# Kernel optimization log

Measured on AMD Instinct MI355X. Metric: run time of the kernel, lower is better.

The kernel has to match this reference:

```python
import jax, jax.numpy as jnp
import numpy as np

LAYERS = 3       # opt.layer
B = 4096         # batch of sessions
MAX_LEN = 200    # padded session length
N_ITEMS = 100000 # item vocab (index 0 is PAD after zero-row concat)
E = 112          # emb_size (SessConv default)
EPS = 1e-12      # F.normalize eps


def setup_inputs() -> dict:
    key = jax.random.key(0)
    k0, k1, k2, k3, k4 = jax.random.split(key, 5)
    item_embedding = jax.random.normal(k0, (N_ITEMS, E), dtype=jnp.float32) * 0.1
    # Session-session adjacency A and diagonal inverse-degree D (so D @ A is row-normalized)
    A = jax.random.uniform(k1, (B, B), dtype=jnp.float32)
    D = jnp.diag(1.0 / A.sum(axis=1))
    # Padded session item indices; 0 == PAD row (zeros prepended to the table)
    session_item = jax.random.randint(k2, (B, MAX_LEN), 0, N_ITEMS + 1, dtype=jnp.int64)
    session_len = jax.random.randint(k3, (B, 1), 1, MAX_LEN + 1).astype(jnp.float32)
    # layers x Linear(E, E, bias=False) weights, torch layout [out, in]
    Ws = jax.random.normal(k4, (LAYERS, E, E), dtype=jnp.float32) * (1.0 / np.sqrt(E))
    return {"item_embedding": item_embedding, "D": D, "A": A,
            "session_len": session_len, "Ws": Ws, "session_item": session_item}


def reference(item_embedding, D, A, session_len, Ws, session_item):
    # Prepend zero row so index 0 gathers zeros (padding)
    emb = jnp.concatenate([jnp.zeros((1, E), item_embedding.dtype), item_embedding], axis=0)
    # Fused ragged gather + mean-pool (replaces per-session index_select + cpu/numpy roundtrip)
    seq_h = emb[session_item]                       # [B, MAX_LEN, E]
    session_emb = seq_h.sum(axis=1) / session_len   # [B, E]
    DA = D @ A                                      # [B, B]
    acc = session_emb                               # layer-0 term of the final average
    for i in range(LAYERS):
        session_emb = session_emb @ Ws[i].T         # Linear(E,E,bias=False)
        session_emb = DA @ session_emb              # session graph propagation
        nrm = jnp.linalg.norm(session_emb, axis=-1, keepdims=True)
        acc = acc + session_emb / jnp.maximum(nrm, EPS)  # appended term is L2-normalized
        # NOTE: next layer consumes the UN-normalized session_emb (as in the torch code)
    return acc / (LAYERS + 1)
```

## Files before the change

### kernel.cpp

```cpp
#include <hip/hip_runtime.h>
#include <hip/hip_bf16.h>

#define BSZ 4096
#define MAXLEN 200
#define EDIM 112
#define NPL 8

typedef __attribute__((ext_vector_type(8))) short bf16x8;
typedef __attribute__((ext_vector_type(4))) float f32x4;

static __device__ __forceinline__ short f2bf(float f) {
    unsigned u = __float_as_uint(f);
    unsigned r = (u + 0x7fffu + ((u >> 16) & 1u)) >> 16;
    return (short)r;
}
static __device__ __forceinline__ float bf2f(short s) {
    return __uint_as_float(((unsigned)(unsigned short)s) << 16);
}
static __device__ __forceinline__ bf16x8 cvt8(float4 a, float4 b) {
    bf16x8 r;
    r[0] = f2bf(a.x); r[1] = f2bf(a.y); r[2] = f2bf(a.z); r[3] = f2bf(a.w);
    r[4] = f2bf(b.x); r[5] = f2bf(b.y); r[6] = f2bf(b.z); r[7] = f2bf(b.w);
    return r;
}
static __device__ __forceinline__ unsigned pack2(float a, float b) {
    return ((unsigned)f2bf(a) & 0xffffu) | ((unsigned)f2bf(b) << 16);
}

static __device__ __forceinline__ void glds16(const unsigned short* g, unsigned short* l) {
    __builtin_amdgcn_global_load_lds(
        (__attribute__((address_space(1))) void*)(void*)g,
        (__attribute__((address_space(3))) void*)l, 16, 0, 0);
}

__global__ __launch_bounds__(256) void f32_to_bf16(const float* __restrict__ src,
                                                   unsigned short* __restrict__ dst,
                                                   int ngroups, int zgroups) {
    int g = blockIdx.x * 256 + threadIdx.x;
    if (g >= ngroups) return;
    bf16x8 o;
    if (g < zgroups) {
        #pragma unroll
        for (int i = 0; i < 8; ++i) o[i] = 0;
    } else {
        const float* p = src + (size_t)(g - zgroups) * 8;
        float4 a = *(const float4*)p;
        float4 b = *(const float4*)(p + 4);
        o = cvt8(a, b);
    }
    *(bf16x8*)(dst + (size_t)g * 8) = o;
}

__global__ __launch_bounds__(256) void gather_pool_bf(const unsigned short* __restrict__ Ebf,
                                                      const int* __restrict__ items,
                                                      const float* __restrict__ slen,
                                                      float* __restrict__ S,
                                                      float* __restrict__ acc) {
    __shared__ float part[16][14][8];
    int wave = threadIdx.x >> 6;
    int lane = threadIdx.x & 63;
    int b = blockIdx.x;
    int rg = lane / 14;
    int c  = lane % 14;
    const int* it = items + (size_t)b * MAXLEN + wave * 50;
    float a[8];
    #pragma unroll
    for (int e = 0; e < 8; ++e) a[e] = 0.f;
    if (lane < 56) {
        #pragma unroll
        for (int t = 0; t < 13; ++t) {
            int j = t * 4 + rg;
            int idx = 0;
            if (j < 50) idx = it[j];
            bf16x8 v = *(const bf16x8*)(Ebf + (size_t)idx * EDIM + c * 8);
            #pragma unroll
            for (int e = 0; e < 8; ++e) a[e] += bf2f(v[e]);
        }
        #pragma unroll
        for (int e = 0; e < 8; ++e) part[wave * 4 + rg][c][e] = a[e];
    }
    __syncthreads();
    int tid = threadIdx.x;
    if (tid < EDIM) {
        int cc = tid >> 3, ee = tid & 7;
        float s = 0.f;
        #pragma unroll
        for (int g = 0; g < 16; ++g) s += part[g][cc][ee];
        s /= slen[b];
        S[(size_t)b * EDIM + tid]   = s;
        acc[(size_t)b * EDIM + tid] = s;
    }
}

static __device__ __forceinline__ bf16x8 ldcvt(const float* p, bool valid) {
    if (valid) {
        float4 a = *(const float4*)(p);
        float4 b = *(const float4*)(p + 4);
        return cvt8(a, b);
    }
    bf16x8 z;
    #pragma unroll
    for (int i = 0; i < 8; ++i) z[i] = 0;
    return z;
}

__global__ __launch_bounds__(64, 4) void fused_mid0(const float* __restrict__ Sin,
                                                    const float* __restrict__ W,
                                                    unsigned short* __restrict__ Bsw) {
    __shared__ unsigned short Ylds[16][136];
    int lane = threadIdx.x;
    int gw = blockIdx.x;
    int j0 = gw * 16;
    int nrow = lane & 15;
    int quad = lane >> 4;
    int ses = j0 + nrow;

    float4 v[7];
    const float4* p = (const float4*)(Sin + (size_t)ses * EDIM + quad * 28);
    #pragma unroll
    for (int i = 0; i < 7; ++i) v[i] = p[i];

    #pragma unroll
    for (int i = 0; i < 7; ++i) {
        uint2 pk;
        pk.x = pack2(v[i].x, v[i].y);
        pk.y = pack2(v[i].z, v[i].w);
        *(uint2*)&Ylds[nrow][quad * 28 + i * 4] = pk;
    }
    *(uint2*)&Ylds[nrow][112 + quad * 4] = make_uint2(0u, 0u);
    __syncthreads();

    bf16x8 aF[4];
    #pragma unroll
    for (int k32 = 0; k32 < 4; ++k32)
        aF[k32] = *(bf16x8*)&Ylds[nrow][k32 * 32 + quad * 8];

    f32x4 acc[7];
    #pragma unroll
    for (int t = 0; t < 7; ++t) acc[t] = (f32x4){0.f, 0.f, 0.f, 0.f};
    #pragma unroll
    for (int t = 0; t < 7; ++t) {
        const float* wr = W + (size_t)(16 * t + nrow) * EDIM;
        #pragma unroll
        for (int k32 = 0; k32 < 4; ++k32) {
            bf16x8 bF = ldcvt(wr + k32 * 32 + quad * 8, (k32 < 3) || (quad < 2));
            acc[t] = __builtin_amdgcn_mfma_f32_16x16x32_bf16(aF[k32], bF, acc[t], 0, 0, 0);
        }
    }

    int k32f = j0 >> 5;
    int qp = ((j0 >> 4) & 1) * 2 + (quad >> 1);
    int e0 = (quad & 1) * 4;
    #pragma unroll
    for (int t = 0; t < 7; ++t) {
        uint2 pk;
        pk.x = pack2(acc[t][0], acc[t][1]);
        pk.y = pack2(acc[t][2], acc[t][3]);
        *(uint2*)(Bsw + ((size_t)(k32f * 7 + t) * 64 + qp * 16 + nrow) * 8 + e0) = pk;
    }
}

template <int AMODE>
__global__ __launch_bounds__(512, 2) void bg_ks(const float* __restrict__ Af,
                                                unsigned short* __restrict__ Asw,
                                                const unsigned short* __restrict__ Bsw,
                                                float* __restrict__ Yp) {
    __shared__ unsigned short Bl[8 * 7 * 512];
    int tid = threadIdx.x;
    int w = tid >> 6;
    int lane = tid & 63;
    int nrow = lane & 15;
    int quad = lane >> 4;
    int mtile = blockIdx.x & 31;
    int kq = blockIdx.x >> 5;
    int M16 = mtile * 8 + w;
    int k32b = kq * 16;

    #pragma unroll
    for (int t = 0; t < 7; ++t)
        glds16(Bsw + (((size_t)(k32b + w) * 7 + t) * 64 + lane) * 8,
               &Bl[(w * 7 + t) * 512]);

    bf16x8 aF[16];
    if (AMODE == 0) {
        #pragma unroll
        for (int k = 0; k < 16; ++k) {
            const float* p = Af + (size_t)(M16 * 16 + nrow) * BSZ
                             + (k32b + k) * 32 + quad * 8;
            float4 a0 = *(const float4*)p;
            float4 a1 = *(const float4*)(p + 4);
            aF[k] = cvt8(a0, a1);
            *(bf16x8*)(Asw + (((size_t)M16 * 128 + k32b + k) * 64 + lane) * 8) = aF[k];
        }
    } else {
        #pragma unroll
        for (int k = 0; k < 16; ++k)
            aF[k] = *(const bf16x8*)(Asw + (((size_t)M16 * 128 + k32b + k) * 64 + lane) * 8);
    }

    f32x4 acc[7];
    #pragma unroll
    for (int t = 0; t < 7; ++t) acc[t] = (f32x4){0.f, 0.f, 0.f, 0.f};

    asm volatile("s_waitcnt vmcnt(0)" ::: "memory");
    __syncthreads();

    #pragma unroll
    for (int k = 0; k < 8; ++k)
        #pragma unroll
        for (int t = 0; t < 7; ++t) {
            bf16x8 bF = *(bf16x8*)&Bl[(k * 7 + t) * 512 + lane * 8];
            acc[t] = __builtin_amdgcn_mfma_f32_16x16x32_bf16(aF[k], bF, acc[t], 0, 0, 0);
        }

    __syncthreads();
    #pragma unroll
    for (int t = 0; t < 7; ++t)
        glds16(Bsw + (((size_t)(k32b + 8 + w) * 7 + t) * 64 + lane) * 8,
               &Bl[(w * 7 + t) * 512]);
    asm volatile("s_waitcnt vmcnt(0)" ::: "memory");
    __syncthreads();

    #pragma unroll
    for (int k = 0; k < 8; ++k)
        #pragma unroll
        for (int t = 0; t < 7; ++t) {
            bf16x8 bF = *(bf16x8*)&Bl[(k * 7 + t) * 512 + lane * 8];
            acc[t] = __builtin_amdgcn_mfma_f32_16x16x32_bf16(aF[8 + k], bF, acc[t], 0, 0, 0);
        }

    float* dst = Yp + (size_t)kq * BSZ * EDIM + (size_t)M16 * 16 * EDIM;
    #pragma unroll
    for (int t = 0; t < 7; ++t)
        #pragma unroll
        for (int r = 0; r < 4; ++r)
            dst[(size_t)(quad * 4 + r) * EDIM + 16 * t + nrow] = acc[t][r];
}

__global__ __launch_bounds__(64, 4) void epi_mid(const float* __restrict__ Yp,
                                                 const float* __restrict__ Dm,
                                                 float* __restrict__ accb,
                                                 const float* __restrict__ W,
                                                 unsigned short* __restrict__ Bsw) {
    __shared__ unsigned short Ylds[16][136];
    int lane = threadIdx.x;
    int gw = blockIdx.x;
    int j0 = gw * 16;
    int nrow = lane & 15;
    int quad = lane >> 4;
    int ses = j0 + nrow;

    float4 v[7];
    #pragma unroll
    for (int i = 0; i < 7; ++i) v[i] = make_float4(0.f, 0.f, 0.f, 0.f);
    #pragma unroll
    for (int pp = 0; pp < NPL; ++pp) {
        const float4* p = (const float4*)(Yp + (size_t)pp * BSZ * EDIM
                                          + (size_t)ses * EDIM + quad * 28);
        #pragma unroll
        for (int i = 0; i < 7; ++i) {
            float4 t = p[i];
            v[i].x += t.x; v[i].y += t.y; v[i].z += t.z; v[i].w += t.w;
        }
    }
    float d = Dm[(size_t)ses * (BSZ + 1)];
    float ss = 0.f;
    #pragma unroll
    for (int i = 0; i < 7; ++i) {
        v[i].x *= d; v[i].y *= d; v[i].z *= d; v[i].w *= d;
        ss += v[i].x * v[i].x + v[i].y * v[i].y + v[i].z * v[i].z + v[i].w * v[i].w;
    }
    ss += __shfl_xor(ss, 16, 64);
    ss += __shfl_xor(ss, 32, 64);
    float rinv = 1.f / fmaxf(sqrtf(ss), 1e-12f);
    float4* pa = (float4*)(accb + (size_t)ses * EDIM + quad * 28);
    #pragma unroll
    for (int i = 0; i < 7; ++i) {
        float4 a = pa[i];
        a.x += v[i].x * rinv; a.y += v[i].y * rinv;
        a.z += v[i].z * rinv; a.w += v[i].w * rinv;
        pa[i] = a;
    }

    #pragma unroll
    for (int i = 0; i < 7; ++i) {
        uint2 pk;
        pk.x = pack2(v[i].x, v[i].y);
        pk.y = pack2(v[i].z, v[i].w);
        *(uint2*)&Ylds[nrow][quad * 28 + i * 4] = pk;
    }
    *(uint2*)&Ylds[nrow][112 + quad * 4] = make_uint2(0u, 0u);
    __syncthreads();

    bf16x8 aF[4];
    #pragma unroll
    for (int k32 = 0; k32 < 4; ++k32)
        aF[k32] = *(bf16x8*)&Ylds[nrow][k32 * 32 + quad * 8];

    f32x4 acc[7];
    #pragma unroll
    for (int t = 0; t < 7; ++t) acc[t] = (f32x4){0.f, 0.f, 0.f, 0.f};
    #pragma unroll
    for (int t = 0; t < 7; ++t) {
        const float* wr = W + (size_t)(16 * t + nrow) * EDIM;
        #pragma unroll
        for (int k32 = 0; k32 < 4; ++k32) {
            bf16x8 bF = ldcvt(wr + k32 * 32 + quad * 8, (k32 < 3) || (quad < 2));
            acc[t] = __builtin_amdgcn_mfma_f32_16x16x32_bf16(aF[k32], bF, acc[t], 0, 0, 0);
        }
    }

    int k32f = j0 >> 5;
    int qp = ((j0 >> 4) & 1) * 2 + (quad >> 1);
    int e0 = (quad & 1) * 4;
    #pragma unroll
    for (int t = 0; t < 7; ++t) {
        uint2 pk;
        pk.x = pack2(acc[t][0], acc[t][1]);
        pk.y = pack2(acc[t][2], acc[t][3]);
        *(uint2*)(Bsw + ((size_t)(k32f * 7 + t) * 64 + qp * 16 + nrow) * 8 + e0) = pk;
    }
}

__global__ __launch_bounds__(256) void final_epilogue(const float* __restrict__ Yp,
                                                      const float* __restrict__ Dm,
                                                      const float* __restrict__ accb,
                                                      float* __restrict__ out) {
    int wave = threadIdx.x >> 6;
    int lane = threadIdx.x & 63;
    int b = blockIdx.x * 4 + wave;

    float2 v = make_float2(0.f, 0.f);
    size_t o2 = (size_t)b * 56 + lane;
    if (lane < 56) {
        #pragma unroll
        for (int p = 0; p < NPL; ++p) {
            float2 t = ((const float2*)(Yp + (size_t)p * BSZ * EDIM))[o2];
            v.x += t.x;
            v.y += t.y;
        }
    }
    float d = Dm[(size_t)b * (BSZ + 1)];
    v.x *= d; v.y *= d;
    float ss = v.x * v.x + v.y * v.y;
    #pragma unroll
    for (int off = 32; off; off >>= 1) ss += __shfl_xor(ss, off, 64);
    float nrm = fmaxf(sqrtf(ss), 1e-12f);
    if (lane < 56) {
        float2 a = ((const float2*)accb)[o2];
        ((float2*)out)[o2] = make_float2((a.x + v.x / nrm) * 0.25f,
                                         (a.y + v.y / nrm) * 0.25f);
    }
}

extern "C" void kernel_launch(void* const* d_in, const int* in_sizes, int n_in,
                              void* d_out, int out_size, void* d_ws, size_t ws_size,
                              hipStream_t stream) {
    (void)in_sizes; (void)n_in; (void)out_size; (void)ws_size;
    const float* emb   = (const float*)d_in[0];
    const float* Dm    = (const float*)d_in[1];
    const float* A     = (const float*)d_in[2];
    const float* slen  = (const float*)d_in[3];
    const float* Ws    = (const float*)d_in[4];
    const int*   items = (const int*)d_in[5];
    float* out = (float*)d_out;

    char* w = (char*)d_ws;
    float* Sa   = (float*)w;
    float* accb = Sa + BSZ * EDIM;
    float* Yp   = accb + BSZ * EDIM;
    unsigned short* Bsw0 = (unsigned short*)(Yp + (size_t)NPL * BSZ * EDIM);
    unsigned short* Bsw1 = Bsw0 + (size_t)128 * 7 * 64 * 8;
    unsigned short* Ebf  = Bsw1 + (size_t)128 * 7 * 64 * 8;
    unsigned short* Asw  = Ebf + (size_t)100001 * EDIM;

    f32_to_bf16<<<5470, 256, 0, stream>>>(emb, Ebf, 1400014, 14);
    gather_pool_bf<<<BSZ, 256, 0, stream>>>(Ebf, items, slen, Sa, accb);
    fused_mid0<<<256, 64, 0, stream>>>(Sa, Ws, Bsw0);
    bg_ks<0><<<256, 512, 0, stream>>>(A, Asw, Bsw0, Yp);
    epi_mid<<<256, 64, 0, stream>>>(Yp, Dm, accb, Ws + (size_t)EDIM * EDIM, Bsw1);
    bg_ks<1><<<256, 512, 0, stream>>>(nullptr, Asw, Bsw1, Yp);
    epi_mid<<<256, 64, 0, stream>>>(Yp, Dm, accb, Ws + (size_t)2 * EDIM * EDIM, Bsw0);
    bg_ks<1><<<256, 512, 0, stream>>>(nullptr, Asw, Bsw0, Yp);
    final_epilogue<<<BSZ / 4, 256, 0, stream>>>(Yp, Dm, accb, out);
}
```

Before: 274.3 us.

## Fuse layer kernels into one persistent kernel with grid-wide atomic barriers

Merges the weight-projection, the three graph-propagation GEMMs, the mid-layer epilogues and the final epilogue into a single persistent kernel of 256 blocks. Stages are separated by a software grid barrier built on an atomic counter. The intent is to remove the launch gaps and the tail idle time between seven small kernels. In exchange it relies on all 256 blocks being co-resident, otherwise it deadlocks, and it adds a memset plus spin-wait overhead at each barrier. The epilogue now runs on one wave per block instead of many small blocks.

```diff
diff --git a/kernel.cpp b/kernel.cpp
--- a/kernel.cpp
+++ b/kernel.cpp
@@ -5,6 +5,7 @@
 #define MAXLEN 200
 #define EDIM 112
 #define NPL 8
+#define NBLK 256
 
 typedef __attribute__((ext_vector_type(8))) short bf16x8;
 typedef __attribute__((ext_vector_type(4))) float f32x4;
@@ -31,6 +32,19 @@
     __builtin_amdgcn_global_load_lds(
         (__attribute__((address_space(1))) void*)(void*)g,
         (__attribute__((address_space(3))) void*)l, 16, 0, 0);
+}
+
+static __device__ __forceinline__ void gsync(unsigned* cnt, unsigned idx) {
+    __syncthreads();
+    if (threadIdx.x == 0) {
+        __threadfence();
+        __hip_atomic_fetch_add(cnt, 1u, __ATOMIC_RELEASE, __HIP_MEMORY_SCOPE_AGENT);
+        while (__hip_atomic_load(cnt, __ATOMIC_ACQUIRE, __HIP_MEMORY_SCOPE_AGENT)
+               < idx * (unsigned)NBLK)
+            __builtin_amdgcn_s_sleep(2);
+        __threadfence();
+    }
+    __syncthreads();
 }
 
 __global__ __launch_bounds__(256) void f32_to_bf16(const float* __restrict__ src,
@@ -104,252 +118,226 @@
     return z;
 }
 
-__global__ __launch_bounds__(64, 4) void fused_mid0(const float* __restrict__ Sin,
-                                                    const float* __restrict__ W,
-                                                    unsigned short* __restrict__ Bsw) {
-    __shared__ unsigned short Ylds[16][136];
-    int lane = threadIdx.x;
-    int gw = blockIdx.x;
-    int j0 = gw * 16;
-    int nrow = lane & 15;
-    int quad = lane >> 4;
-    int ses = j0 + nrow;
-
-    float4 v[7];
-    const float4* p = (const float4*)(Sin + (size_t)ses * EDIM + quad * 28);
-    #pragma unroll
-    for (int i = 0; i < 7; ++i) v[i] = p[i];
-
-    #pragma unroll
-    for (int i = 0; i < 7; ++i) {
-        uint2 pk;
-        pk.x = pack2(v[i].x, v[i].y);
-        pk.y = pack2(v[i].z, v[i].w);
-        *(uint2*)&Ylds[nrow][quad * 28 + i * 4] = pk;
-    }
-    *(uint2*)&Ylds[nrow][112 + quad * 4] = make_uint2(0u, 0u);
-    __syncthreads();
-
-    bf16x8 aF[4];
-    #pragma unroll
-    for (int k32 = 0; k32 < 4; ++k32)
-        aF[k32] = *(bf16x8*)&Ylds[nrow][k32 * 32 + quad * 8];
-
-    f32x4 acc[7];
-    #pragma unroll
-    for (int t = 0; t < 7; ++t) acc[t] = (f32x4){0.f, 0.f, 0.f, 0.f};
-    #pragma unroll
-    for (int t = 0; t < 7; ++t) {
-        const float* wr = W + (size_t)(16 * t + nrow) * EDIM;
-        #pragma unroll
-        for (int k32 = 0; k32 < 4; ++k32) {
-            bf16x8 bF = ldcvt(wr + k32 * 32 + quad * 8, (k32 < 3) || (quad < 2));
-            acc[t] = __builtin_amdgcn_mfma_f32_16x16x32_bf16(aF[k32], bF, acc[t], 0, 0, 0);
-        }
-    }
-
-    int k32f = j0 >> 5;
-    int qp = ((j0 >> 4) & 1) * 2 + (quad >> 1);
-    int e0 = (quad & 1) * 4;
-    #pragma unroll
-    for (int t = 0; t < 7; ++t) {
-        uint2 pk;
-        pk.x = pack2(acc[t][0], acc[t][1]);
-        pk.y = pack2(acc[t][2], acc[t][3]);
-        *(uint2*)(Bsw + ((size_t)(k32f * 7 + t) * 64 + qp * 16 + nrow) * 8 + e0) = pk;
-    }
-}
-
-template <int AMODE>
-__global__ __launch_bounds__(512, 2) void bg_ks(const float* __restrict__ Af,
-                                                unsigned short* __restrict__ Asw,
-                                                const unsigned short* __restrict__ Bsw,
-                                                float* __restrict__ Yp) {
-    __shared__ unsigned short Bl[8 * 7 * 512];
+__global__ __launch_bounds__(512, 2) void mega(const float* __restrict__ Af,
+                                               unsigned short* __restrict__ Asw,
+                                               const float* __restrict__ Sin,
+                                               const float* __restrict__ Dm,
+                                               float* __restrict__ accb,
+                                               const float* __restrict__ Ws,
+                                               unsigned short* __restrict__ Bsw0,
+                                               unsigned short* __restrict__ Bsw1,
+                                               float* __restrict__ Yp,
+                                               float* __restrict__ out,
+                                               unsigned* __restrict__ cnt) {
+    __shared__ alignas(16) char smem[57344];
     int tid = threadIdx.x;
     int w = tid >> 6;
     int lane = tid & 63;
     int nrow = lane & 15;
     int quad = lane >> 4;
-    int mtile = blockIdx.x & 31;
-    int kq = blockIdx.x >> 5;
-    int M16 = mtile * 8 + w;
-    int k32b = kq * 16;
-
-    #pragma unroll
-    for (int t = 0; t < 7; ++t)
-        glds16(Bsw + (((size_t)(k32b + w) * 7 + t) * 64 + lane) * 8,
-               &Bl[(w * 7 + t) * 512]);
-
-    bf16x8 aF[16];
-    if (AMODE == 0) {
-        #pragma unroll
-        for (int k = 0; k < 16; ++k) {
-            const float* p = Af + (size_t)(M16 * 16 + nrow) * BSZ
-                             + (k32b + k) * 32 + quad * 8;
-            float4 a0 = *(const float4*)p;
-            float4 a1 = *(const float4*)(p + 4);
-            aF[k] = cvt8(a0, a1);
-            *(bf16x8*)(Asw + (((size_t)M16 * 128 + k32b + k) * 64 + lane) * 8) = aF[k];
-        }
-    } else {
-        #pragma unroll
-        for (int k = 0; k < 16; ++k)
-            aF[k] = *(const bf16x8*)(Asw + (((size_t)M16 * 128 + k32b + k) * 64 + lane) * 8);
-    }
-
-    f32x4 acc[7];
-    #pragma unroll
-    for (int t = 0; t < 7; ++t) acc[t] = (f32x4){0.f, 0.f, 0.f, 0.f};
-
-    asm volatile("s_waitcnt vmcnt(0)" ::: "memory");
-    __syncthreads();
-
-    #pragma unroll
-    for (int k = 0; k < 8; ++k)
+    int b = blockIdx.x;
+
+    if (w == 0) {
+        unsigned short (*Ylds)[136] = (unsigned short(*)[136])smem;
+        int j0 = b * 16;
+        int ses = j0 + nrow;
+        float4 v[7];
+        const float4* p = (const float4*)(Sin + (size_t)ses * EDIM + quad * 28);
+        #pragma unroll
+        for (int i = 0; i < 7; ++i) v[i] = p[i];
+        #pragma unroll
+        for (int i = 0; i < 7; ++i) {
+            uint2 pk;
+            pk.x = pack2(v[i].x, v[i].y);
+            pk.y = pack2(v[i].z, v[i].w);
+            *(uint2*)&Ylds[nrow][quad * 28 + i * 4] = pk;
+        }
+        *(uint2*)&Ylds[nrow][112 + quad * 4] = make_uint2(0u, 0u);
+        __builtin_amdgcn_s_waitcnt(0);
+        bf16x8 aF[4];
+        #pragma unroll
+        for (int k = 0; k < 4; ++k)
+            aF[k] = *(bf16x8*)&Ylds[nrow][k * 32 + quad * 8];
+        f32x4 acc[7];
+        #pragma unroll
+        for (int t = 0; t < 7; ++t) acc[t] = (f32x4){0.f, 0.f, 0.f, 0.f};
         #pragma unroll
         for (int t = 0; t < 7; ++t) {
-            bf16x8 bF = *(bf16x8*)&Bl[(k * 7 + t) * 512 + lane * 8];
-            acc[t] = __builtin_amdgcn_mfma_f32_16x16x32_bf16(aF[k], bF, acc[t], 0, 0, 0);
-        }
-
-    __syncthreads();
-    #pragma unroll
-    for (int t = 0; t < 7; ++t)
-        glds16(Bsw + (((size_t)(k32b + 8 + w) * 7 + t) * 64 + lane) * 8,
-               &Bl[(w * 7 + t) * 512]);
-    asm volatile("s_waitcnt vmcnt(0)" ::: "memory");
-    __syncthreads();
-
-    #pragma unroll
-    for (int k = 0; k < 8; ++k)
+            const float* wr = Ws + (size_t)(16 * t + nrow) * EDIM;
+            #pragma unroll
+            for (int k = 0; k < 4; ++k) {
+                bf16x8 bF = ldcvt(wr + k * 32 + quad * 8, (k < 3) || (quad < 2));
+                acc[t] = __builtin_amdgcn_mfma_f32_16x16x32_bf16(aF[k], bF, acc[t], 0, 0, 0);
+            }
+        }
+        int k32f = j0 >> 5;
+        int qp = ((j0 >> 4) & 1) * 2 + (quad >> 1);
+        int e0 = (quad & 1) * 4;
         #pragma unroll
         for (int t = 0; t < 7; ++t) {
-            bf16x8 bF = *(bf16x8*)&Bl[(k * 7 + t) * 512 + lane * 8];
-            acc[t] = __builtin_amdgcn_mfma_f32_16x16x32_bf16(aF[8 + k], bF, acc[t], 0, 0, 0);
-        }
-
-    float* dst = Yp + (size_t)kq * BSZ * EDIM + (size_t)M16 * 16 * EDIM;
-    #pragma unroll
-    for (int t = 0; t < 7; ++t)
-        #pragma unroll
-        for (int r = 0; r < 4; ++r)
-            dst[(size_t)(quad * 4 + r) * EDIM + 16 * t + nrow] = acc[t][r];
-}
-
-__global__ __launch_bounds__(64, 4) void epi_mid(const float* __restrict__ Yp,
-                                                 const float* __restrict__ Dm,
-                                                 float* __restrict__ accb,
-                                                 const float* __restrict__ W,
-                                                 unsigned short* __restrict__ Bsw) {
-    __shared__ unsigned short Ylds[16][136];
-    int lane = threadIdx.x;
-    int gw = blockIdx.x;
-    int j0 = gw * 16;
-    int nrow = lane & 15;
-    int quad = lane >> 4;
-    int ses = j0 + nrow;
-
-    float4 v[7];
-    #pragma unroll
-    for (int i = 0; i < 7; ++i) v[i] = make_float4(0.f, 0.f, 0.f, 0.f);
-    #pragma unroll
-    for (int pp = 0; pp < NPL; ++pp) {
-        const float4* p = (const float4*)(Yp + (size_t)pp * BSZ * EDIM
-                                          + (size_t)ses * EDIM + quad * 28);
-        #pragma unroll
-        for (int i = 0; i < 7; ++i) {
-            float4 t = p[i];
-            v[i].x += t.x; v[i].y += t.y; v[i].z += t.z; v[i].w += t.w;
-        }
-    }
-    float d = Dm[(size_t)ses * (BSZ + 1)];
-    float ss = 0.f;
-    #pragma unroll
-    for (int i = 0; i < 7; ++i) {
-        v[i].x *= d; v[i].y *= d; v[i].z *= d; v[i].w *= d;
-        ss += v[i].x * v[i].x + v[i].y * v[i].y + v[i].z * v[i].z + v[i].w * v[i].w;
-    }
-    ss += __shfl_xor(ss, 16, 64);
-    ss += __shfl_xor(ss, 32, 64);
-    float rinv = 1.f / fmaxf(sqrtf(ss), 1e-12f);
-    float4* pa = (float4*)(accb + (size_t)ses * EDIM + quad * 28);
-    #pragma unroll
-    for (int i = 0; i < 7; ++i) {
-        float4 a = pa[i];
-        a.x += v[i].x * rinv; a.y += v[i].y * rinv;
-        a.z += v[i].z * rinv; a.w += v[i].w * rinv;
-        pa[i] = a;
-    }
-
-    #pragma unroll
-    for (int i = 0; i < 7; ++i) {
-        uint2 pk;
-        pk.x = pack2(v[i].x, v[i].y);
-        pk.y = pack2(v[i].z, v[i].w);
-        *(uint2*)&Ylds[nrow][quad * 28 + i * 4] = pk;
-    }
-    *(uint2*)&Ylds[nrow][112 + quad * 4] = make_uint2(0u, 0u);
-    __syncthreads();
-
-    bf16x8 aF[4];
-    #pragma unroll
-    for (int k32 = 0; k32 < 4; ++k32)
-        aF[k32] = *(bf16x8*)&Ylds[nrow][k32 * 32 + quad * 8];
-
-    f32x4 acc[7];
-    #pragma unroll
-    for (int t = 0; t < 7; ++t) acc[t] = (f32x4){0.f, 0.f, 0.f, 0.f};
-    #pragma unroll
-    for (int t = 0; t < 7; ++t) {
-        const float* wr = W + (size_t)(16 * t + nrow) * EDIM;
-        #pragma unroll
-        for (int k32 = 0; k32 < 4; ++k32) {
-            bf16x8 bF = ldcvt(wr + k32 * 32 + quad * 8, (k32 < 3) || (quad < 2));
-            acc[t] = __builtin_amdgcn_mfma_f32_16x16x32_bf16(aF[k32], bF, acc[t], 0, 0, 0);
-        }
-    }
-
-    int k32f = j0 >> 5;
-    int qp = ((j0 >> 4) & 1) * 2 + (quad >> 1);
-    int e0 = (quad & 1) * 4;
-    #pragma unroll
-    for (int t = 0; t < 7; ++t) {
-        uint2 pk;
-        pk.x = pack2(acc[t][0], acc[t][1]);
-        pk.y = pack2(acc[t][2], acc[t][3]);
-        *(uint2*)(Bsw + ((size_t)(k32f * 7 + t) * 64 + qp * 16 + nrow) * 8 + e0) = pk;
-    }
-}
-
-__global__ __launch_bounds__(256) void final_epilogue(const float* __restrict__ Yp,
-                                                      const float* __restrict__ Dm,
-                                                      const float* __restrict__ accb,
-                                                      float* __restrict__ out) {
-    int wave = threadIdx.x >> 6;
-    int lane = threadIdx.x & 63;
-    int b = blockIdx.x * 4 + wave;
-
-    float2 v = make_float2(0.f, 0.f);
-    size_t o2 = (size_t)b * 56 + lane;
-    if (lane < 56) {
-        #pragma unroll
-        for (int p = 0; p < NPL; ++p) {
-            float2 t = ((const float2*)(Yp + (size_t)p * BSZ * EDIM))[o2];
-            v.x += t.x;
-            v.y += t.y;
-        }
-    }
-    float d = Dm[(size_t)b * (BSZ + 1)];
-    v.x *= d; v.y *= d;
-    float ss = v.x * v.x + v.y * v.y;
-    #pragma unroll
-    for (int off = 32; off; off >>= 1) ss += __shfl_xor(ss, off, 64);
-    float nrm = fmaxf(sqrtf(ss), 1e-12f);
-    if (lane < 56) {
-        float2 a = ((const float2*)accb)[o2];
-        ((float2*)out)[o2] = make_float2((a.x + v.x / nrm) * 0.25f,
-                                         (a.y + v.y / nrm) * 0.25f);
+            uint2 pk;
+            pk.x = pack2(acc[t][0], acc[t][1]);
+            pk.y = pack2(acc[t][2], acc[t][3]);
+            *(uint2*)(Bsw0 + ((size_t)(k32f * 7 + t) * 64 + qp * 16 + nrow) * 8 + e0) = pk;
+        }
+    }
+    gsync(cnt, 1);
+
+    #pragma unroll 1
+    for (int l = 0; l < 3; ++l) {
+        {
+            unsigned short* Bl = (unsigned short*)smem;
+            const unsigned short* BswIn = (l == 1) ? Bsw1 : Bsw0;
+            int mtile = b & 31;
+            int kq = b >> 5;
+            int M16 = mtile * 8 + w;
+            int k32b = kq * 16;
+
+            #pragma unroll
+            for (int t = 0; t < 7; ++t)
+                glds16(BswIn + (((size_t)(k32b + w) * 7 + t) * 64 + lane) * 8,
+                       &Bl[(w * 7 + t) * 512]);
+
+            bf16x8 aF[16];
+            if (l == 0) {
+                #pragma unroll
+                for (int k = 0; k < 16; ++k) {
+                    const float* p = Af + (size_t)(M16 * 16 + nrow) * BSZ
+                                     + (k32b + k) * 32 + quad * 8;
+                    float4 a0 = *(const float4*)p;
+                    float4 a1 = *(const float4*)(p + 4);
+                    aF[k] = cvt8(a0, a1);
+                    *(bf16x8*)(Asw + (((size_t)M16 * 128 + k32b + k) * 64 + lane) * 8) = aF[k];
+                }
+            } else {
+                #pragma unroll
+                for (int k = 0; k < 16; ++k)
+                    aF[k] = *(const bf16x8*)(Asw + (((size_t)M16 * 128 + k32b + k) * 64 + lane) * 8);
+            }
+
+            f32x4 acc[7];
+            #pragma unroll
+            for (int t = 0; t < 7; ++t) acc[t] = (f32x4){0.f, 0.f, 0.f, 0.f};
+
+            asm volatile("s_waitcnt vmcnt(0)" ::: "memory");
+            __syncthreads();
+            #pragma unroll
+            for (int k = 0; k < 8; ++k)
+                #pragma unroll
+                for (int t = 0; t < 7; ++t) {
+                    bf16x8 bF = *(bf16x8*)&Bl[(k * 7 + t) * 512 + lane * 8];
+                    acc[t] = __builtin_amdgcn_mfma_f32_16x16x32_bf16(aF[k], bF, acc[t], 0, 0, 0);
+                }
+            __syncthreads();
+            #pragma unroll
+            for (int t = 0; t < 7; ++t)
+                glds16(BswIn + (((size_t)(k32b + 8 + w) * 7 + t) * 64 + lane) * 8,
+                       &Bl[(w * 7 + t) * 512]);
+            asm volatile("s_waitcnt vmcnt(0)" ::: "memory");
+            __syncthreads();
+            #pragma unroll
+            for (int k = 0; k < 8; ++k)
+                #pragma unroll
+                for (int t = 0; t < 7; ++t) {
+                    bf16x8 bF = *(bf16x8*)&Bl[(k * 7 + t) * 512 + lane * 8];
+                    acc[t] = __builtin_amdgcn_mfma_f32_16x16x32_bf16(aF[8 + k], bF, acc[t], 0, 0, 0);
+                }
+
+            float* dst = Yp + (size_t)kq * BSZ * EDIM + (size_t)M16 * 16 * EDIM;
+            #pragma unroll
+            for (int t = 0; t < 7; ++t)
+                #pragma unroll
+                for (int r = 0; r < 4; ++r)
+                    dst[(size_t)(quad * 4 + r) * EDIM + 16 * t + nrow] = acc[t][r];
+        }
+        gsync(cnt, 2 + 2 * l);
+
+        {
+            float4* Yred = (float4*)smem;
+            unsigned short (*Ylds)[136] = (unsigned short(*)[136])(smem + 7168);
+            if (tid < 448) {
+                int row = tid / 28;
+                int c4 = tid - row * 28;
+                float4 s = make_float4(0.f, 0.f, 0.f, 0.f);
+                #pragma unroll
+                for (int pp = 0; pp < NPL; ++pp) {
+                    float4 t = *(const float4*)(Yp + (size_t)pp * BSZ * EDIM
+                                                + (size_t)(b * 16 + row) * EDIM + c4 * 4);
+                    s.x += t.x; s.y += t.y; s.z += t.z; s.w += t.w;
+                }
+                Yred[row * 28 + c4] = s;
+            }
+            __syncthreads();
+            if (w == 0) {
+                float4 v[7];
+                #pragma unroll
+                for (int i = 0; i < 7; ++i) v[i] = Yred[nrow * 28 + quad * 7 + i];
+                float d = Dm[(size_t)(b * 16 + nrow) * (BSZ + 1)];
+                float ss = 0.f;
+                #pragma unroll
+                for (int i = 0; i < 7; ++i) {
+                    v[i].x *= d; v[i].y *= d; v[i].z *= d; v[i].w *= d;
+                    ss += v[i].x * v[i].x + v[i].y * v[i].y
+                        + v[i].z * v[i].z + v[i].w * v[i].w;
+                }
+                ss += __shfl_xor(ss, 16, 64);
+                ss += __shfl_xor(ss, 32, 64);
+                float rinv = 1.f / fmaxf(sqrtf(ss), 1e-12f);
+                if (l == 2) {
+                    #pragma unroll
+                    for (int i = 0; i < 7; ++i) {
+                        size_t o = (size_t)(b * 16 + nrow) * EDIM + quad * 28 + i * 4;
+                        float4 a = *(const float4*)(accb + o);
+                        float4 r;
+                        r.x = (a.x + v[i].x * rinv) * 0.25f;
+                        r.y = (a.y + v[i].y * rinv) * 0.25f;
+                        r.z = (a.z + v[i].z * rinv) * 0.25f;
+                        r.w = (a.w + v[i].w * rinv) * 0.25f;
+                        *(float4*)(out + o) = r;
+                    }
+                } else {
+                    #pragma unroll
+                    for (int i = 0; i < 7; ++i) {
+                        size_t o = (size_t)(b * 16 + nrow) * EDIM + quad * 28 + i * 4;
+                        float4 a = *(const float4*)(accb + o);
+                        a.x += v[i].x * rinv; a.y += v[i].y * rinv;
+                        a.z += v[i].z * rinv; a.w += v[i].w * rinv;
+                        *(float4*)(accb + o) = a;
+                        uint2 pk;
+                        pk.x = pack2(v[i].x, v[i].y);
+                        pk.y = pack2(v[i].z, v[i].w);
+                        *(uint2*)&Ylds[nrow][quad * 28 + i * 4] = pk;
+                    }
+                    *(uint2*)&Ylds[nrow][112 + quad * 4] = make_uint2(0u, 0u);
+                    __builtin_amdgcn_s_waitcnt(0);
+                    bf16x8 aF2[4];
+                    #pragma unroll
+                    for (int k = 0; k < 4; ++k)
+                        aF2[k] = *(bf16x8*)&Ylds[nrow][k * 32 + quad * 8];
+                    const float* Wn = Ws + (size_t)(l + 1) * EDIM * EDIM;
+                    unsigned short* BswOut = (l == 0) ? Bsw1 : Bsw0;
+                    int j0 = b * 16;
+                    int k32f = j0 >> 5;
+                    int qp = ((j0 >> 4) & 1) * 2 + (quad >> 1);
+                    int e0 = (quad & 1) * 4;
+                    #pragma unroll
+                    for (int t = 0; t < 7; ++t) {
+                        f32x4 c = (f32x4){0.f, 0.f, 0.f, 0.f};
+                        const float* wr = Wn + (size_t)(16 * t + nrow) * EDIM;
+                        #pragma unroll
+                        for (int k = 0; k < 4; ++k) {
+                            bf16x8 bW = ldcvt(wr + k * 32 + quad * 8, (k < 3) || (quad < 2));
+                            c = __builtin_amdgcn_mfma_f32_16x16x32_bf16(aF2[k], bW, c, 0, 0, 0);
+                        }
+                        uint2 ck;
+                        ck.x = pack2(c[0], c[1]);
+                        ck.y = pack2(c[2], c[3]);
+                        *(uint2*)(BswOut + ((size_t)(k32f * 7 + t) * 64 + qp * 16 + nrow) * 8 + e0) = ck;
+                    }
+                }
+            }
+        }
+        if (l < 2) gsync(cnt, 3 + 2 * l);
     }
 }
 
@@ -373,14 +361,11 @@
     unsigned short* Bsw1 = Bsw0 + (size_t)128 * 7 * 64 * 8;
     unsigned short* Ebf  = Bsw1 + (size_t)128 * 7 * 64 * 8;
     unsigned short* Asw  = Ebf + (size_t)100001 * EDIM;
-
+    unsigned* cnt = (unsigned*)(Asw + (size_t)BSZ * BSZ);
+
+    hipMemsetAsync(cnt, 0, 64, stream);
     f32_to_bf16<<<5470, 256, 0, stream>>>(emb, Ebf, 1400014, 14);
     gather_pool_bf<<<BSZ, 256, 0, stream>>>(Ebf, items, slen, Sa, accb);
-    fused_mid0<<<256, 64, 0, stream>>>(Sa, Ws, Bsw0);
-    bg_ks<0><<<256, 512, 0, stream>>>(A, Asw, Bsw0, Yp);
-    epi_mid<<<256, 64, 0, stream>>>(Yp, Dm, accb, Ws + (size_t)EDIM * EDIM, Bsw1);
-    bg_ks<1><<<256, 512, 0, stream>>>(nullptr, Asw, Bsw1, Yp);
-    epi_mid<<<256, 64, 0, stream>>>(Yp, Dm, accb, Ws + (size_t)2 * EDIM * EDIM, Bsw0);
-    bg_ks<1><<<256, 512, 0, stream>>>(nullptr, Asw, Bsw0, Yp);
-    final_epilogue<<<BSZ / 4, 256, 0, stream>>>(Yp, Dm, accb, out);
-}
+    mega<<<NBLK, 512, 0, stream>>>(A, Asw, Sa, Dm, accb, Ws,
+                                   Bsw0, Bsw1, Yp, out, cnt);
+}
```

New measurement: 426.9 us. 1.56x slower.
